# Kernel optimization log

Hardware: AMD Instinct MI355X
Metric: run time of the kernel (lower is better)

## Reference

```python
import jax, jax.numpy as jnp
import numpy as np

DECAY = 0.9


def setup_inputs() -> dict:
    key = jax.random.key(0)
    ks = jax.random.split(key, 8)
    B, L, d_model = 4, 2048, 1024
    d_state = 16
    d_inner = 2 * d_model  # expand=2
    x = jax.random.normal(ks[0], (B, L, d_model), dtype=jnp.float32)
    Win = jax.random.normal(ks[1], (d_model, d_inner), dtype=jnp.float32) / np.sqrt(d_model)
    bin_ = jnp.zeros((d_inner,), dtype=jnp.float32)
    Bp = jax.random.normal(ks[2], (d_inner, d_state), dtype=jnp.float32) * 0.01
    Cp = jax.random.normal(ks[3], (d_state, d_inner), dtype=jnp.float32) * 0.01
    Dp = jnp.ones((d_inner,), dtype=jnp.float32)
    Wout = jax.random.normal(ks[4], (d_inner, d_model), dtype=jnp.float32) / np.sqrt(d_inner)
    bout = jnp.zeros((d_model,), dtype=jnp.float32)
    return {"x": x, "Win": Win, "bin_": bin_, "Bp": Bp, "Cp": Cp, "Dp": Dp,
            "Wout": Wout, "bout": bout}


def reference(x, Win, bin_, Bp, Cp, Dp, Wout, bout):
    # x: [B, L, d_model]
    B, L, _ = x.shape
    d_inner, d_state = Bp.shape
    xi = jax.nn.silu(x @ Win + bin_)          # [B, L, d_inner]
    xt_seq = jnp.swapaxes(xi, 0, 1)            # [L, B, d_inner] for scan over time

    def step(h, xt):
        # h: [B, d_inner, d_state]; xt: [B, d_inner]
        h = h * DECAY + xt[:, :, None] * Bp[None, :, :]
        y = jnp.einsum('bij,ji->bi', h, Cp) + Dp * xt
        return h, y

    h0 = jnp.zeros((B, d_inner, d_state), dtype=x.dtype)
    _, ys = jax.lax.scan(step, h0, xt_seq)     # ys: [L, B, d_inner]
    y = jnp.swapaxes(ys, 0, 1)                 # [B, L, d_inner]
    return y @ Wout + bout                     # [B, L, d_model]
```

## Files before the change

### kernel.cpp

```cpp
#include <hip/hip_runtime.h>
#include <hip/hip_bf16.h>
#include <cstdint>
#include <cstddef>

typedef __attribute__((ext_vector_type(8))) short short8_t;
typedef __attribute__((ext_vector_type(4))) float f32x4;

__device__ __forceinline__ void gload16(const void* g, void* l) {
  __builtin_amdgcn_global_load_lds(
      (const __attribute__((address_space(1))) void*)g,
      (__attribute__((address_space(3))) void*)l, 16, 0, 0);
}

#define BARRIER() do { asm volatile("" ::: "memory"); __builtin_amdgcn_s_barrier(); asm volatile("" ::: "memory"); } while (0)
#define LGKM0 asm volatile("s_waitcnt lgkmcnt(0)" ::: "memory")
#define WVM(n) asm volatile("s_waitcnt vmcnt(" #n ")" ::: "memory")

__global__ __launch_bounds__(256) void cvt_bf16_kernel(
    const float* __restrict__ in, __hip_bfloat16* __restrict__ out, int n) {
  int gid = blockIdx.x * blockDim.x + threadIdx.x;
  int idx = gid * 4;
  if (idx >= n) return;
  float4 v = *reinterpret_cast<const float4*>(in + idx);
  union { short4 s4; __hip_bfloat16 h[4]; } u;
  u.h[0] = __float2bfloat16(v.x);
  u.h[1] = __float2bfloat16(v.y);
  u.h[2] = __float2bfloat16(v.z);
  u.h[3] = __float2bfloat16(v.w);
  *reinterpret_cast<short4*>(out + idx) = u.s4;
}

__global__ __launch_bounds__(256) void transpose_cvt_kernel(
    const float* __restrict__ in, __hip_bfloat16* __restrict__ out, int R, int C) {
  __shared__ float tile[32][33];
  int c0 = blockIdx.x * 32, r0 = blockIdx.y * 32;
  int tx = threadIdx.x, ty = threadIdx.y;
#pragma unroll
  for (int j = 0; j < 32; j += 8)
    tile[ty + j][tx] = in[(size_t)(r0 + ty + j) * C + c0 + tx];
  __syncthreads();
#pragma unroll
  for (int j = 0; j < 32; j += 8)
    out[(size_t)(c0 + ty + j) * R + r0 + tx] = __float2bfloat16(tile[tx][ty + j]);
}

template <int EPI>
__global__ __launch_bounds__(256, 3) void gemm_cr_kernel(
    const __hip_bfloat16* __restrict__ A,
    const __hip_bfloat16* __restrict__ Bt,
    const float* __restrict__ bias,
    void* __restrict__ Cout,
    int M, int N, int K) {
  constexpr int AUNIT = 8192, BUNIT = 8192;
  constexpr int BOFF = 3 * AUNIT;
  __shared__ int4 ldsv[(3 * AUNIT + 3 * BUNIT) / 16];
  char* lds = (char*)ldsv;

  const int tid = threadIdx.x;
  const int l = tid & 63;
  const int w = tid >> 6;
  const int wm = w >> 1, wn = w & 1;
  const int fr = l & 15;
  const int sl = ((l >> 4) ^ ((fr >> 3) << 1)) * 16;
  const int arowb = (wm * 64 + fr) * 64 + sl;
  const int browb = (wn * 64 + fr) * 64 + sl;

  const int nbn = N / 128;
  int bid = blockIdx.x;
  const int cpx = gridDim.x >> 3;
  bid = (bid & 7) * cpx + (bid >> 3);
  const int brow = (bid / nbn) * 128;
  const int bcol = (bid % nbn) * 128;
  const size_t K2 = (size_t)K * 2;

  int ar[2], acb[2], dst[2];
#pragma unroll
  for (int j = 0; j < 2; ++j) {
    int d = j * 4096 + tid * 16;
    int lg = d ^ (((d >> 9) & 1) << 5);
    ar[j] = lg >> 6;  acb[j] = lg & 63;
    dst[j] = j * 4096 + w * 1024;
  }

  const char* Abp = (const char*)A;
  const char* Bbp = (const char*)Bt;

  auto stAB = [&](int t, int buf) {
    const int ab = buf * AUNIT;
#pragma unroll
    for (int j = 0; j < 2; ++j)
      gload16(Abp + (size_t)(brow + ar[j]) * K2 + t * 64 + acb[j], lds + ab + dst[j]);
    const int bb = BOFF + buf * BUNIT;
#pragma unroll
    for (int j = 0; j < 2; ++j)
      gload16(Bbp + (size_t)(bcol + ar[j]) * K2 + t * 64 + acb[j], lds + bb + dst[j]);
  };

  f32x4 acc[4][4];
#pragma unroll
  for (int m = 0; m < 4; ++m)
#pragma unroll
    for (int n = 0; n < 4; ++n) acc[m][n] = (f32x4)0.f;

  const int NT = K >> 5;
  stAB(0, 0); stAB(1, 1);
  WVM(4); BARRIER();

  int cur = 0, stg = 2;
  for (int T = 0; T < NT; ++T) {
    if (T + 2 < NT) stAB(T + 2, stg);
    short8_t af[4], bf[4];
    const int ab = cur * AUNIT, bb = BOFF + cur * BUNIT;
#pragma unroll
    for (int mi = 0; mi < 4; ++mi)
      af[mi] = *(const short8_t*)(lds + ab + arowb + mi * 1024);
#pragma unroll
    for (int n = 0; n < 4; ++n)
      bf[n] = *(const short8_t*)(lds + bb + browb + n * 1024);
#pragma unroll
    for (int mi = 0; mi < 4; ++mi)
#pragma unroll
      for (int n = 0; n < 4; ++n)
        acc[mi][n] = __builtin_amdgcn_mfma_f32_16x16x32_bf16(af[mi], bf[n], acc[mi][n], 0, 0, 0);
    if (T + 1 < NT) {
      if (T + 2 < NT) { WVM(4); } else { WVM(0); }
      LGKM0;
      BARRIER();
    }
    cur = (cur == 2) ? 0 : cur + 1;
    stg = (stg == 2) ? 0 : stg + 1;
  }

  const int r0 = brow + wm * 64 + (l >> 4) * 4;
  const int c0 = bcol + wn * 64 + fr;
#pragma unroll
  for (int m = 0; m < 4; ++m) {
#pragma unroll
    for (int n = 0; n < 4; ++n) {
      const int col = c0 + n * 16;
      const float bv = bias[col];
#pragma unroll
      for (int j = 0; j < 4; ++j) {
        const int row = r0 + m * 16 + j;
        float v = acc[m][n][j] + bv;
        if constexpr (EPI == 0) {
          v = v / (1.0f + __expf(-v));
          ((__hip_bfloat16*)Cout)[(size_t)row * N + col] = __float2bfloat16(v);
        } else {
          ((float*)Cout)[(size_t)row * N + col] = v;
        }
      }
    }
  }
}

__global__ __launch_bounds__(256) void scan_kernel(
    const __hip_bfloat16* __restrict__ xi,
    const float* __restrict__ Bp,
    const float* __restrict__ Cp,
    const float* __restrict__ Dp,
    __hip_bfloat16* __restrict__ y) {
  constexpr int L = 2048, DI = 2048, DS = 16, TW = 256, H = 32;
  const int tid = threadIdx.x;
  const int bidx = blockIdx.x;
  const int iblk = bidx & 7;
  const int chunk = (bidx >> 3) & 7;
  const int b = bidx >> 6;
  const int i = iblk * 256 + tid;

  float cb = 0.f;
#pragma unroll
  for (int s = 0; s < DS; ++s) cb += Bp[i * DS + s] * Cp[s * DI + i];
  const float dp = Dp[i];

  const int t0 = chunk * TW;
  int tstart = t0 - H;
  if (tstart < 0) tstart = 0;

  const __hip_bfloat16* xp = xi + (size_t)(b * L) * DI + i;
  __hip_bfloat16* yp = y + (size_t)(b * L) * DI + i;

  float g = 0.f;
  const __hip_bfloat16* p = xp + (size_t)tstart * DI;
  for (int t = tstart; t < t0; ++t, p += DI)
    g = g * 0.9f + __bfloat162float(*p);
  __hip_bfloat16* q = yp + (size_t)t0 * DI;
  for (int t = 0; t < TW; ++t, p += DI, q += DI) {
    float xv = __bfloat162float(*p);
    g = g * 0.9f + xv;
    *q = __float2bfloat16(cb * g + dp * xv);
  }
}

extern "C" void kernel_launch(void* const* d_in, const int* in_sizes, int n_in,
                              void* d_out, int out_size, void* d_ws, size_t ws_size,
                              hipStream_t stream) {
  const float* x    = (const float*)d_in[0];
  const float* Win  = (const float*)d_in[1];
  const float* bin  = (const float*)d_in[2];
  const float* Bp   = (const float*)d_in[3];
  const float* Cp   = (const float*)d_in[4];
  const float* Dp   = (const float*)d_in[5];
  const float* Wout = (const float*)d_in[6];
  const float* bout = (const float*)d_in[7];
  float* out = (float*)d_out;

  constexpr int Bb = 4, L = 2048, DM = 1024, DI = 2048;
  constexpr int Mrows = Bb * L;

  char* ws = (char*)d_ws;
  __hip_bfloat16* xb    = (__hip_bfloat16*)ws;
  __hip_bfloat16* WinT  = (__hip_bfloat16*)(ws + (16u << 20));
  __hip_bfloat16* WoutT = (__hip_bfloat16*)(ws + (20u << 20));
  __hip_bfloat16* xi    = (__hip_bfloat16*)(ws + (24u << 20));
  __hip_bfloat16* yb    = (__hip_bfloat16*)(ws + (56u << 20));

  {
    int n = Mrows * DM;
    cvt_bf16_kernel<<<n / 1024, 256, 0, stream>>>(x, xb, n);
  }
  transpose_cvt_kernel<<<dim3(DI / 32, DM / 32), dim3(32, 8), 0, stream>>>(Win, WinT, DM, DI);
  transpose_cvt_kernel<<<dim3(DM / 32, DI / 32), dim3(32, 8), 0, stream>>>(Wout, WoutT, DI, DM);
  gemm_cr_kernel<0><<<(Mrows / 128) * (DI / 128), 256, 0, stream>>>(
      xb, WinT, bin, (void*)xi, Mrows, DI, DM);
  scan_kernel<<<Bb * (L / 256) * (DI / 256), 256, 0, stream>>>(xi, Bp, Cp, Dp, yb);
  gemm_cr_kernel<1><<<(Mrows / 128) * (DM / 128), 256, 0, stream>>>(
      yb, WoutT, bout, (void*)out, Mrows, DM, DI);
}
```

Measured before the change: 133.0 us.

## Use 256x128 GEMM tiles with 512 threads and six-stage LDS pipeline

The GEMM block grows from 128x128 with 256 threads to 256x128 with 512 threads (8 waves, each still 64x64). The LDS ring goes from three stages to six, and the loop processes two K-tiles per barrier, issuing two prefetches four tiles ahead. This doubles B-tile reuse per block, halves the number of barriers, and deepens the prefetch to hide global latency. In exchange it uses about 144KB of LDS and allows only one block per CU, so occupancy drops.

```diff
diff --git a/kernel.cpp b/kernel.cpp
--- a/kernel.cpp
+++ b/kernel.cpp
@@ -45,15 +45,15 @@
 }
 
 template <int EPI>
-__global__ __launch_bounds__(256, 3) void gemm_cr_kernel(
+__global__ __launch_bounds__(512, 1) void gemm6b_kernel(
     const __hip_bfloat16* __restrict__ A,
     const __hip_bfloat16* __restrict__ Bt,
     const float* __restrict__ bias,
     void* __restrict__ Cout,
     int M, int N, int K) {
-  constexpr int AUNIT = 8192, BUNIT = 8192;
-  constexpr int BOFF = 3 * AUNIT;
-  __shared__ int4 ldsv[(3 * AUNIT + 3 * BUNIT) / 16];
+  constexpr int AUNIT = 16384, BUNIT = 8192;
+  constexpr int BOFF = 6 * AUNIT;
+  __shared__ int4 ldsv[(6 * AUNIT + 6 * BUNIT) / 16];
   char* lds = (char*)ldsv;
 
   const int tid = threadIdx.x;
@@ -62,38 +62,39 @@
   const int wm = w >> 1, wn = w & 1;
   const int fr = l & 15;
   const int sl = ((l >> 4) ^ ((fr >> 3) << 1)) * 16;
-  const int arowb = (wm * 64 + fr) * 64 + sl;
-  const int browb = (wn * 64 + fr) * 64 + sl;
+  const int arow_base = (wm * 64 + fr) * 64 + sl;
+  const int brow_base = (wn * 64 + fr) * 64 + sl;
 
   const int nbn = N / 128;
   int bid = blockIdx.x;
   const int cpx = gridDim.x >> 3;
   bid = (bid & 7) * cpx + (bid >> 3);
-  const int brow = (bid / nbn) * 128;
+  const int brow = (bid / nbn) * 256;
   const int bcol = (bid % nbn) * 128;
   const size_t K2 = (size_t)K * 2;
 
-  int ar[2], acb[2], dst[2];
+  int arA[2], acbA[2], dstA[2];
 #pragma unroll
   for (int j = 0; j < 2; ++j) {
-    int d = j * 4096 + tid * 16;
+    int d = j * 8192 + tid * 16;
     int lg = d ^ (((d >> 9) & 1) << 5);
-    ar[j] = lg >> 6;  acb[j] = lg & 63;
-    dst[j] = j * 4096 + w * 1024;
-  }
+    arA[j] = lg >> 6;  acbA[j] = lg & 63;
+    dstA[j] = j * 8192 + w * 1024;
+  }
+  int dB = tid * 16;
+  int lgB = dB ^ (((dB >> 9) & 1) << 5);
+  const int arB = lgB >> 6, acbB = lgB & 63, dstB = w * 1024;
 
   const char* Abp = (const char*)A;
   const char* Bbp = (const char*)Bt;
 
-  auto stAB = [&](int t, int buf) {
-    const int ab = buf * AUNIT;
+  auto stT = [&](int t, int buf) {
 #pragma unroll
     for (int j = 0; j < 2; ++j)
-      gload16(Abp + (size_t)(brow + ar[j]) * K2 + t * 64 + acb[j], lds + ab + dst[j]);
-    const int bb = BOFF + buf * BUNIT;
-#pragma unroll
-    for (int j = 0; j < 2; ++j)
-      gload16(Bbp + (size_t)(bcol + ar[j]) * K2 + t * 64 + acb[j], lds + bb + dst[j]);
+      gload16(Abp + (size_t)(brow + arA[j]) * K2 + (size_t)t * 64 + acbA[j],
+              lds + buf * AUNIT + dstA[j]);
+    gload16(Bbp + (size_t)(bcol + arB) * K2 + (size_t)t * 64 + acbB,
+            lds + BOFF + buf * BUNIT + dstB);
   };
 
   f32x4 acc[4][4];
@@ -102,33 +103,42 @@
 #pragma unroll
     for (int n = 0; n < 4; ++n) acc[m][n] = (f32x4)0.f;
 
-  const int NT = K >> 5;
-  stAB(0, 0); stAB(1, 1);
-  WVM(4); BARRIER();
-
-  int cur = 0, stg = 2;
-  for (int T = 0; T < NT; ++T) {
-    if (T + 2 < NT) stAB(T + 2, stg);
+  auto tilework = [&](int buf) {
     short8_t af[4], bf[4];
-    const int ab = cur * AUNIT, bb = BOFF + cur * BUNIT;
 #pragma unroll
     for (int mi = 0; mi < 4; ++mi)
-      af[mi] = *(const short8_t*)(lds + ab + arowb + mi * 1024);
+      af[mi] = *(const short8_t*)(lds + buf * AUNIT + arow_base + mi * 1024);
 #pragma unroll
     for (int n = 0; n < 4; ++n)
-      bf[n] = *(const short8_t*)(lds + bb + browb + n * 1024);
+      bf[n] = *(const short8_t*)(lds + BOFF + buf * BUNIT + brow_base + n * 1024);
 #pragma unroll
     for (int mi = 0; mi < 4; ++mi)
 #pragma unroll
       for (int n = 0; n < 4; ++n)
         acc[mi][n] = __builtin_amdgcn_mfma_f32_16x16x32_bf16(af[mi], bf[n], acc[mi][n], 0, 0, 0);
-    if (T + 1 < NT) {
-      if (T + 2 < NT) { WVM(4); } else { WVM(0); }
+  };
+
+  const int NT = K >> 5;
+  const int NS = NT >> 1;
+  stT(0, 0); stT(1, 1); stT(2, 2); stT(3, 3);
+  WVM(6); BARRIER();
+
+  int cur = 0;
+  for (int S = 0; S < NS; ++S) {
+    const int T = 2 * S;
+    const int s4 = (cur + 4 >= 6) ? cur - 2 : cur + 4;
+    const int s5 = (cur + 5 >= 6) ? cur - 1 : cur + 5;
+    if (T + 4 < NT) stT(T + 4, s4);
+    tilework(cur);
+    if (T + 5 < NT) stT(T + 5, s5);
+    const int nxt = (cur + 1 >= 6) ? 0 : cur + 1;
+    tilework(nxt);
+    if (S + 1 < NS) {
+      if (T + 4 < NT) { WVM(6); } else { WVM(0); }
       LGKM0;
       BARRIER();
     }
-    cur = (cur == 2) ? 0 : cur + 1;
-    stg = (stg == 2) ? 0 : stg + 1;
+    cur = (cur + 2 >= 6) ? cur - 4 : cur + 2;
   }
 
   const int r0 = brow + wm * 64 + (l >> 4) * 4;
@@ -221,9 +231,9 @@
   }
   transpose_cvt_kernel<<<dim3(DI / 32, DM / 32), dim3(32, 8), 0, stream>>>(Win, WinT, DM, DI);
   transpose_cvt_kernel<<<dim3(DM / 32, DI / 32), dim3(32, 8), 0, stream>>>(Wout, WoutT, DI, DM);
-  gemm_cr_kernel<0><<<(Mrows / 128) * (DI / 128), 256, 0, stream>>>(
+  gemm6b_kernel<0><<<(Mrows / 256) * (DI / 128), 512, 0, stream>>>(
       xb, WinT, bin, (void*)xi, Mrows, DI, DM);
   scan_kernel<<<Bb * (L / 256) * (DI / 256), 256, 0, stream>>>(xi, Bp, Cp, Dp, yb);
-  gemm_cr_kernel<1><<<(Mrows / 128) * (DM / 128), 256, 0, stream>>>(
+  gemm6b_kernel<1><<<(Mrows / 256) * (DM / 128), 512, 0, stream>>>(
       yb, WoutT, bout, (void*)out, Mrows, DM, DI);
 }
```

New measurement: 132.9 us. No clear change (-0.1%).

## Enlarge GEMM tiles to 256x128 with 512 threads and K=64 stages

Applied to the files above, without the earlier changes.

Replaces the 128x128 GEMM with a 256x128 tile computed by 8 waves (512 threads), and deepens each K step from 32 to 64 with a new XOR swizzle for the 128-byte LDS rows. All fragments are now read from LDS before the next stage's global loads are issued. The aim is more reuse of the B tile per block and fewer barriers per unit of K. It costs much more LDS (144 KB for the triple buffer) and more registers, which limits occupancy, and the grid becomes half as large.

```diff
diff --git a/kernel.cpp b/kernel.cpp
--- a/kernel.cpp
+++ b/kernel.cpp
@@ -45,13 +45,13 @@
 }
 
 template <int EPI>
-__global__ __launch_bounds__(256, 3) void gemm_cr_kernel(
+__global__ __launch_bounds__(512, 2) void gemm_seg_kernel(
     const __hip_bfloat16* __restrict__ A,
     const __hip_bfloat16* __restrict__ Bt,
     const float* __restrict__ bias,
     void* __restrict__ Cout,
     int M, int N, int K) {
-  constexpr int AUNIT = 8192, BUNIT = 8192;
+  constexpr int AUNIT = 32768, BUNIT = 16384;
   constexpr int BOFF = 3 * AUNIT;
   __shared__ int4 ldsv[(3 * AUNIT + 3 * BUNIT) / 16];
   char* lds = (char*)ldsv;
@@ -61,39 +61,40 @@
   const int w = tid >> 6;
   const int wm = w >> 1, wn = w & 1;
   const int fr = l & 15;
-  const int sl = ((l >> 4) ^ ((fr >> 3) << 1)) * 16;
-  const int arowb = (wm * 64 + fr) * 64 + sl;
-  const int browb = (wn * 64 + fr) * 64 + sl;
+  const int q16 = (l >> 4) * 16;
+  const int swz = (fr & 7) << 4;
+  const int arow_base = (wm * 64 + fr) * 128;
+  const int brow_base = (wn * 64 + fr) * 128;
 
   const int nbn = N / 128;
   int bid = blockIdx.x;
   const int cpx = gridDim.x >> 3;
   bid = (bid & 7) * cpx + (bid >> 3);
-  const int brow = (bid / nbn) * 128;
+  const int brow = (bid / nbn) * 256;
   const int bcol = (bid % nbn) * 128;
   const size_t K2 = (size_t)K * 2;
 
-  int ar[2], acb[2], dst[2];
-#pragma unroll
-  for (int j = 0; j < 2; ++j) {
-    int d = j * 4096 + tid * 16;
-    int lg = d ^ (((d >> 9) & 1) << 5);
-    ar[j] = lg >> 6;  acb[j] = lg & 63;
-    dst[j] = j * 4096 + w * 1024;
+  int srow[4], scol[4], dstw[4];
+#pragma unroll
+  for (int j = 0; j < 4; ++j) {
+    int d = j * 8192 + tid * 16;
+    int lg = d ^ (((d >> 7) & 7) << 4);
+    srow[j] = lg >> 7;  scol[j] = lg & 127;
+    dstw[j] = j * 8192 + w * 1024;
   }
 
   const char* Abp = (const char*)A;
   const char* Bbp = (const char*)Bt;
 
-  auto stAB = [&](int t, int buf) {
-    const int ab = buf * AUNIT;
+  auto stT = [&](int t, int ab) {
+#pragma unroll
+    for (int j = 0; j < 4; ++j)
+      gload16(Abp + (size_t)(brow + srow[j]) * K2 + (size_t)t * 128 + scol[j],
+              lds + ab + dstw[j]);
 #pragma unroll
     for (int j = 0; j < 2; ++j)
-      gload16(Abp + (size_t)(brow + ar[j]) * K2 + t * 64 + acb[j], lds + ab + dst[j]);
-    const int bb = BOFF + buf * BUNIT;
-#pragma unroll
-    for (int j = 0; j < 2; ++j)
-      gload16(Bbp + (size_t)(bcol + ar[j]) * K2 + t * 64 + acb[j], lds + bb + dst[j]);
+      gload16(Bbp + (size_t)(bcol + srow[j]) * K2 + (size_t)t * 128 + scol[j],
+              lds + BOFF + ab / 2 + dstw[j]);
   };
 
   f32x4 acc[4][4];
@@ -102,33 +103,39 @@
 #pragma unroll
     for (int n = 0; n < 4; ++n) acc[m][n] = (f32x4)0.f;
 
-  const int NT = K >> 5;
-  stAB(0, 0); stAB(1, 1);
-  WVM(4); BARRIER();
-
-  int cur = 0, stg = 2;
+  const int NT = K >> 6;
+  stT(0, 0); stT(1, AUNIT);
+  WVM(6); BARRIER();
+
+  int curA = 0, stAb = 2 * AUNIT;
   for (int T = 0; T < NT; ++T) {
-    if (T + 2 < NT) stAB(T + 2, stg);
-    short8_t af[4], bf[4];
-    const int ab = cur * AUNIT, bb = BOFF + cur * BUNIT;
-#pragma unroll
-    for (int mi = 0; mi < 4; ++mi)
-      af[mi] = *(const short8_t*)(lds + ab + arowb + mi * 1024);
-#pragma unroll
-    for (int n = 0; n < 4; ++n)
-      bf[n] = *(const short8_t*)(lds + bb + browb + n * 1024);
-#pragma unroll
-    for (int mi = 0; mi < 4; ++mi)
+    short8_t af[8], bf[8];
+#pragma unroll
+    for (int kh = 0; kh < 2; ++kh) {
+      const int ko = (kh * 64 + q16) ^ swz;
+#pragma unroll
+      for (int mi = 0; mi < 4; ++mi)
+        af[kh * 4 + mi] = *(const short8_t*)(lds + curA + arow_base + mi * 2048 + ko);
 #pragma unroll
       for (int n = 0; n < 4; ++n)
-        acc[mi][n] = __builtin_amdgcn_mfma_f32_16x16x32_bf16(af[mi], bf[n], acc[mi][n], 0, 0, 0);
+        bf[kh * 4 + n] = *(const short8_t*)(lds + BOFF + curA / 2 + brow_base + n * 2048 + ko);
+    }
+    if (T + 2 < NT) stT(T + 2, stAb);
+#pragma unroll
+    for (int kh = 0; kh < 2; ++kh)
+#pragma unroll
+      for (int mi = 0; mi < 4; ++mi)
+#pragma unroll
+        for (int n = 0; n < 4; ++n)
+          acc[mi][n] = __builtin_amdgcn_mfma_f32_16x16x32_bf16(
+              af[kh * 4 + mi], bf[kh * 4 + n], acc[mi][n], 0, 0, 0);
     if (T + 1 < NT) {
-      if (T + 2 < NT) { WVM(4); } else { WVM(0); }
+      if (T + 2 < NT) { WVM(6); } else { WVM(0); }
       LGKM0;
       BARRIER();
     }
-    cur = (cur == 2) ? 0 : cur + 1;
-    stg = (stg == 2) ? 0 : stg + 1;
+    curA += AUNIT; if (curA == 3 * AUNIT) curA = 0;
+    stAb += AUNIT; if (stAb == 3 * AUNIT) stAb = 0;
   }
 
   const int r0 = brow + wm * 64 + (l >> 4) * 4;
@@ -221,9 +228,9 @@
   }
   transpose_cvt_kernel<<<dim3(DI / 32, DM / 32), dim3(32, 8), 0, stream>>>(Win, WinT, DM, DI);
   transpose_cvt_kernel<<<dim3(DM / 32, DI / 32), dim3(32, 8), 0, stream>>>(Wout, WoutT, DI, DM);
-  gemm_cr_kernel<0><<<(Mrows / 128) * (DI / 128), 256, 0, stream>>>(
+  gemm_seg_kernel<0><<<(Mrows / 256) * (DI / 128), 512, 0, stream>>>(
       xb, WinT, bin, (void*)xi, Mrows, DI, DM);
   scan_kernel<<<Bb * (L / 256) * (DI / 256), 256, 0, stream>>>(xi, Bp, Cp, Dp, yb);
-  gemm_cr_kernel<1><<<(Mrows / 128) * (DM / 128), 256, 0, stream>>>(
+  gemm_seg_kernel<1><<<(Mrows / 256) * (DM / 128), 512, 0, stream>>>(
       yb, WoutT, bout, (void*)out, Mrows, DM, DI);
 }
```

Result: faster. 129.0 us (-3.0%).
